# Optimization experiments

Measured on AMD Instinct MI355X. Metric: run time of the kernel, lower is better.

## Reference

```python
import jax, jax.numpy as jnp
import numpy as np

B, N, D_MODEL = 16, 65536, 512
NBUCKETS = 11
BN_EPS = 1e-5
LN_EPS = 1e-5


def setup_inputs() -> dict:
    key = jax.random.key(0)
    ks = jax.random.split(key, 12)
    def w(k, shape, fan_in):
        return jax.random.normal(k, shape, jnp.float32) * (1.0 / np.sqrt(fan_in))
    return {
        "x": jax.random.normal(ks[0], (B, N, 3), jnp.float32),
        "w1": w(ks[1], (3, 64), 3),   "b1": jnp.zeros((64,), jnp.float32),
        "g1": jnp.ones((64,), jnp.float32),  "be1": jnp.zeros((64,), jnp.float32),
        "w2": w(ks[2], (64, 128), 64), "b2": jnp.zeros((128,), jnp.float32),
        "g2": jnp.ones((128,), jnp.float32), "be2": jnp.zeros((128,), jnp.float32),
        "w3": w(ks[3], (128, 256), 128), "b3": jnp.zeros((256,), jnp.float32),
        "g3": jnp.ones((256,), jnp.float32), "be3": jnp.zeros((256,), jnp.float32),
        "wp": w(ks[4], (518, D_MODEL), 518), "bp": jnp.zeros((D_MODEL,), jnp.float32),
        "g_ln": jnp.ones((D_MODEL,), jnp.float32), "b_ln": jnp.zeros((D_MODEL,), jnp.float32),
    }


def _bn(h, g, b):
    # BatchNorm1d in training mode: biased variance over the flattened batch axis
    m = jnp.mean(h, axis=0)
    v = jnp.mean((h - m) ** 2, axis=0)
    return (h - m) * jax.lax.rsqrt(v + BN_EPS) * g + b


def reference(x, w1, b1, g1, be1, w2, b2, g2, be2, w3, b3, g3, be3, wp, bp, g_ln, b_ln):
    Bb, Nn, _ = x.shape
    x_flat = x.reshape(Bb * Nn, 3)
    h = jax.nn.relu(_bn(x_flat @ w1 + b1, g1, be1))
    h = jax.nn.relu(_bn(h @ w2 + b2, g2, be2))
    h = jax.nn.relu(_bn(h @ w3 + b3, g3, be3))
    feat = h.reshape(Bb, Nn, 256)

    # y-bucket histogram means of (x, z) coordinates, vectorized via segment_sum
    y = x[:, :, 1]
    y_min = jnp.min(y, axis=1, keepdims=True)
    y_max = jnp.max(y, axis=1, keepdims=True)
    y_norm = (y - y_min) / (y_max - y_min + 1e-6)
    buckets = jnp.clip((y_norm * 10).astype(jnp.int32), 0, NBUCKETS - 1)  # (B,N) in [0,10]
    seg = (jnp.arange(Bb, dtype=jnp.int32)[:, None] * NBUCKETS + buckets).reshape(-1)
    nseg = Bb * NBUCKETS
    sx = jax.ops.segment_sum(x[:, :, 0].reshape(-1), seg, num_segments=nseg)
    sz = jax.ops.segment_sum(x[:, :, 2].reshape(-1), seg, num_segments=nseg)
    cnt = jax.ops.segment_sum(jnp.ones((Bb * Nn,), jnp.float32), seg, num_segments=nseg)
    denom = jnp.maximum(cnt, 1.0)
    cx = (sx / denom).reshape(Bb, NBUCKETS)
    cz = (sz / denom).reshape(Bb, NBUCKETS)
    x_centers = jnp.take_along_axis(cx, buckets, axis=1)  # (B,N)
    z_centers = jnp.take_along_axis(cz, buckets, axis=1)

    dx = x[:, :, 0] - x_centers
    dz = x[:, :, 2] - z_centers
    theta = jnp.arctan2(dz, dx)
    r = jnp.sqrt(dx ** 2 + dz ** 2)
    spatial = jnp.stack([jnp.sin(theta), jnp.cos(theta), r], axis=-1)  # (B,N,3)

    feat = jnp.concatenate([feat, spatial], axis=-1)  # (B,N,259)
    feat_max = jnp.max(feat, axis=1)
    feat_avg = jnp.mean(feat, axis=1)
    feat_cat = jnp.concatenate([feat_max, feat_avg], axis=1)  # (B,518)

    out = feat_cat @ wp + bp
    mu = jnp.mean(out, axis=-1, keepdims=True)
    var = jnp.mean((out - mu) ** 2, axis=-1, keepdims=True)
    return (out - mu) * jax.lax.rsqrt(var + LN_EPS) * g_ln + b_ln
```

## Files before the change

kernel.cpp:

```cpp
#include <hip/hip_runtime.h>
#include <stdint.h>

#define B_    16
#define N_    65536
#define NPTS  (B_*N_)
#define NBK   11
#define NFEAT 259
#define NF    ((float)NPTS)

typedef float f32x4 __attribute__((ext_vector_type(4)));
typedef short s16x8 __attribute__((ext_vector_type(8)));

enum {
  OFF_YMINF = 16,
  OFF_YMAXF = 32,
  OFF_A1    = 64,
  OFF_C1    = 128,
  OFF_A2    = 192,
  OFF_C2    = 320,
  OFF_CX    = 448,
  OFF_CZ    = 624,
  OFF_A3    = 800,
  OFF_C3    = 1056,
  OFF_PSTR  = 16384,
  OFF_PBKT  = 24576,
  OFF_PH2   = 49152,
  OFF_PH3   = 311296,
  OFF_PPOOL = 835584,
  OFF_PSPA  = 1359872
};

__device__ __forceinline__ float wave_sum(float v){
  #pragma unroll
  for (int m=32;m>=1;m>>=1) v += __shfl_xor(v,m,64);
  return v;
}
__device__ __forceinline__ float wave_max(float v){
  #pragma unroll
  for (int m=32;m>=1;m>>=1) v = fmaxf(v,__shfl_xor(v,m,64));
  return v;
}
__device__ __forceinline__ float wave_min(float v){
  #pragma unroll
  for (int m=32;m>=1;m>>=1) v = fminf(v,__shfl_xor(v,m,64));
  return v;
}
__device__ __forceinline__ unsigned short bf16_bits(float f){
  unsigned u=__float_as_uint(f);
  u += 0x7FFFu + ((u>>16)&1u);
  return (unsigned short)(u>>16);
}

__global__ __launch_bounds__(256) void k_stream0(const float* __restrict__ x,
                                                 float* __restrict__ ws){
  __shared__ float red[4][12];
  const int t=threadIdx.x, l=t&63, w=t>>6;
  const int bid=blockIdx.x;
  const float4* xv=(const float4*)(x + (size_t)bid*2048*3);
  float s0=0,s1=0,s2=0,q00=0,q01=0,q02=0,q11=0,q12=0,q22=0;
  float ymn=3.4e38f, ymx=-3.4e38f;
  #pragma unroll
  for (int i=0;i<2;i++){
    const int vi=(i*256+t)*3;
    const float4 a=xv[vi], b4=xv[vi+1], c=xv[vi+2];
    float X[4]={a.x,a.w,b4.z,c.y};
    float Y[4]={a.y,b4.x,b4.w,c.z};
    float Z[4]={a.z,b4.y,c.x,c.w};
    #pragma unroll
    for (int p=0;p<4;p++){
      s0+=X[p]; s1+=Y[p]; s2+=Z[p];
      q00=fmaf(X[p],X[p],q00); q01=fmaf(X[p],Y[p],q01); q02=fmaf(X[p],Z[p],q02);
      q11=fmaf(Y[p],Y[p],q11); q12=fmaf(Y[p],Z[p],q12); q22=fmaf(Z[p],Z[p],q22);
      ymn=fminf(ymn,Y[p]); ymx=fmaxf(ymx,Y[p]);
    }
  }
  s0=wave_sum(s0); s1=wave_sum(s1); s2=wave_sum(s2);
  q00=wave_sum(q00); q01=wave_sum(q01); q02=wave_sum(q02);
  q11=wave_sum(q11); q12=wave_sum(q12); q22=wave_sum(q22);
  ymn=wave_min(ymn); ymx=wave_max(ymx);
  if (l==0){
    red[w][0]=s0; red[w][1]=s1; red[w][2]=s2;
    red[w][3]=q00; red[w][4]=q01; red[w][5]=q02;
    red[w][6]=q11; red[w][7]=q12; red[w][8]=q22;
    red[w][9]=ymn; red[w][10]=ymx;
  }
  __syncthreads();
  if (t<11){
    const float v0=red[0][t],v1=red[1][t],v2=red[2][t],v3=red[3][t];
    float r;
    if (t==9)       r=fminf(fminf(v0,v1),fminf(v2,v3));
    else if (t==10) r=fmaxf(fmaxf(v0,v1),fmaxf(v2,v3));
    else            r=v0+v1+v2+v3;
    ws[OFF_PSTR+bid*16+t]=r;
  }
}

__global__ void k_finA(const float* __restrict__ w1, const float* __restrict__ b1,
                       const float* __restrict__ gm, const float* __restrict__ bt,
                       float* __restrict__ ws){
  __shared__ float sums[9];
  const int t=threadIdx.x;
  if (t<9){
    float s=0.f;
    #pragma unroll 8
    for (int blk=0;blk<512;blk++) s+=ws[OFF_PSTR+blk*16+t];
    sums[t]=s;
  }
  if (t>=32&&t<48){
    const int b=t-32; float m=3.4e38f;
    #pragma unroll 8
    for (int blk=0;blk<32;blk++) m=fminf(m,ws[OFF_PSTR+(b*32+blk)*16+9]);
    ws[OFF_YMINF+b]=m;
  }
  if (t>=48&&t<64){
    const int b=t-48; float m=-3.4e38f;
    #pragma unroll 8
    for (int blk=0;blk<32;blk++) m=fmaxf(m,ws[OFF_PSTR+(b*32+blk)*16+10]);
    ws[OFF_YMAXF+b]=m;
  }
  __syncthreads();
  if (t<64){
    const float i_n=1.f/NF;
    const float w0=w1[t], wa=w1[64+t], wb=w1[128+t];
    const float ms=(w0*sums[0]+wa*sums[1]+wb*sums[2])*i_n;
    const float es=(w0*w0*sums[3]+wa*wa*sums[6]+wb*wb*sums[8]
                   +2.f*(w0*wa*sums[4]+w0*wb*sums[5]+wa*wb*sums[7]))*i_n;
    const float var=es-ms*ms;
    const float a=gm[t]/sqrtf(var+1e-5f);
    ws[OFF_A1+t]=a; ws[OFF_C1+t]=bt[t]-(ms+b1[t])*a;
  }
}

__global__ __launch_bounds__(256) void k_bucket(const float* __restrict__ x,
                                                float* __restrict__ ws){
  __shared__ float red[4][12];
  const int t=threadIdx.x, l=t&63, w=t>>6;
  const int bid=blockIdx.x, b=bid>>5;
  const float ymn=ws[OFF_YMINF+b], ymx=ws[OFF_YMAXF+b];
  const float4* xv=(const float4*)(x + (size_t)bid*2048*3);
  float sxl[NBK], szl[NBK], cntl[NBK];
  #pragma unroll
  for (int k=0;k<NBK;k++){ sxl[k]=0.f; szl[k]=0.f; cntl[k]=0.f; }
  #pragma unroll
  for (int i=0;i<2;i++){
    const int vi=(i*256+t)*3;
    const float4 a=xv[vi], b4=xv[vi+1], c=xv[vi+2];
    float X[4]={a.x,a.w,b4.z,c.y};
    float Y[4]={a.y,b4.x,b4.w,c.z};
    float Z[4]={a.z,b4.y,c.x,c.w};
    #pragma unroll
    for (int p=0;p<4;p++){
      const float yn=(Y[p]-ymn)/(ymx-ymn+1e-6f);
      int bk=(int)(yn*10.f); bk = bk<0?0:(bk>10?10:bk);
      #pragma unroll
      for (int k=0;k<NBK;k++){
        const bool m=(bk==k);
        sxl[k]+= m?X[p]:0.f; szl[k]+= m?Z[p]:0.f; cntl[k]+= m?1.f:0.f;
      }
    }
  }
  #pragma unroll
  for (int k=0;k<NBK;k++){
    const float s=wave_sum(sxl[k]);
    if (l==0) red[w][k]=s;
  }
  __syncthreads();
  if (t<NBK) ws[OFF_PBKT+bid*36+t]=red[0][t]+red[1][t]+red[2][t]+red[3][t];
  __syncthreads();
  #pragma unroll
  for (int k=0;k<NBK;k++){
    const float z=wave_sum(szl[k]);
    if (l==0) red[w][k]=z;
  }
  __syncthreads();
  if (t<NBK) ws[OFF_PBKT+bid*36+11+t]=red[0][t]+red[1][t]+red[2][t]+red[3][t];
  __syncthreads();
  #pragma unroll
  for (int k=0;k<NBK;k++){
    const float c=wave_sum(cntl[k]);
    if (l==0) red[w][k]=c;
  }
  __syncthreads();
  if (t<NBK) ws[OFF_PBKT+bid*36+22+t]=red[0][t]+red[1][t]+red[2][t]+red[3][t];
}

__global__ void k_finB(const float* __restrict__ gm, const float* __restrict__ bt,
                       float* __restrict__ ws){
  __shared__ float acc[256];
  const int t=threadIdx.x;
  {
    const int col=t&127, part=t>>7;
    float s=0.f;
    #pragma unroll 8
    for (int blk=0;blk<1024;blk++) s+=ws[OFF_PH2+blk*256+part*128+col];
    acc[t]=s;
  }
  __syncthreads();
  if (t<128){
    const float i_n=1.f/NF;
    const float m=acc[t]*i_n;
    const float v=acc[128+t]*i_n-m*m;
    const float a=gm[t]/sqrtf(v+1e-5f);
    ws[OFF_A2+t]=a; ws[OFF_C2+t]=bt[t]-m*a;
  }
  if (t<176){
    const int b=t/NBK, k=t-b*NBK;
    float sx=0.f, sz=0.f, cn=0.f;
    #pragma unroll 8
    for (int blk=0;blk<32;blk++){
      const int p=OFF_PBKT+(b*32+blk)*36;
      sx+=ws[p+k]; sz+=ws[p+11+k]; cn+=ws[p+22+k];
    }
    const float d=fmaxf(cn,1.f);
    ws[OFF_CX+t]=sx/d; ws[OFF_CZ+t]=sz/d;
  }
}

__global__ void k_finC(const float* __restrict__ gm, const float* __restrict__ bt,
                       float* __restrict__ ws){
  __shared__ float acc[512];
  const int t=threadIdx.x;
  {
    const int col=t&255, part=t>>8;
    float s=0.f;
    #pragma unroll 8
    for (int blk=0;blk<1024;blk++) s+=ws[OFF_PH3+blk*512+part*256+col];
    acc[t]=s;
  }
  __syncthreads();
  if (t<256){
    const float i_n=1.f/NF;
    const float m=acc[t]*i_n;
    const float v=acc[256+t]*i_n-m*m;
    const float a=gm[t]/sqrtf(v+1e-5f);
    ws[OFF_A3+t]=a; ws[OFF_C3+t]=bt[t]-m*a;
  }
}

__global__ __launch_bounds__(256) void k_spatial(const float* __restrict__ x,
                                                 float* __restrict__ ws){
  __shared__ float red[4][8];
  const int t=threadIdx.x, l=t&63, w=t>>6;
  const int bid=blockIdx.x, b=bid>>5;
  const float ymn=ws[OFF_YMINF+b], ymx=ws[OFF_YMAXF+b];
  const float4* xv=(const float4*)(x + (size_t)bid*2048*3);
  float mx[3]={-3.4e38f,-3.4e38f,-3.4e38f}, sm[3]={0.f,0.f,0.f};
  #pragma unroll
  for (int i=0;i<2;i++){
    const int vi=(i*256+t)*3;
    const float4 a=xv[vi], b4=xv[vi+1], c=xv[vi+2];
    float X[4]={a.x,a.w,b4.z,c.y};
    float Y[4]={a.y,b4.x,b4.w,c.z};
    float Z[4]={a.z,b4.y,c.x,c.w};
    #pragma unroll
    for (int p=0;p<4;p++){
      const float yn=(Y[p]-ymn)/(ymx-ymn+1e-6f);
      int bk=(int)(yn*10.f); bk = bk<0?0:(bk>10?10:bk);
      const float dx=X[p]-ws[OFF_CX+b*NBK+bk];
      const float dz=Z[p]-ws[OFF_CZ+b*NBK+bk];
      const float r=sqrtf(fmaf(dx,dx,dz*dz));
      const float sn=(r>0.f)?(dz/r):0.f;
      const float cs=(r>0.f)?(dx/r):1.f;
      mx[0]=fmaxf(mx[0],sn); sm[0]+=sn;
      mx[1]=fmaxf(mx[1],cs); sm[1]+=cs;
      mx[2]=fmaxf(mx[2],r);  sm[2]+=r;
    }
  }
  #pragma unroll
  for (int q=0;q<3;q++){
    const float m=wave_max(mx[q]);
    const float s=wave_sum(sm[q]);
    if (l==0){ red[w][q]=m; red[w][4+q]=s; }
  }
  __syncthreads();
  if (t<3)        ws[OFF_PSPA+bid*8+t]  =fmaxf(fmaxf(red[0][t],red[1][t]),fmaxf(red[2][t],red[3][t]));
  else if (t>=4&&t<7){
    const int q=t-4;
    ws[OFF_PSPA+bid*8+4+q]=red[0][4+q]+red[1][4+q]+red[2][4+q]+red[3][4+q];
  }
}

template<int MODE>
__global__ __launch_bounds__(512,1) void k_mlp(
    const float* __restrict__ x,
    const float* __restrict__ w1, const float* __restrict__ b1,
    const float* __restrict__ w2, const float* __restrict__ b2,
    const float* __restrict__ w3, const float* __restrict__ b3,
    float* __restrict__ ws)
{
  __shared__ short g1t[128*72];
  __shared__ short g2t[128*136];
  const int t=threadIdx.x, w=t>>6, l=t&63, lg=l>>4, lr=l&15;
  const int bid=blockIdx.x, b=bid>>5, chunk=bid&31;
  const int ptg=w&1, fgrp=w>>1;
  char* g1c=(char*)g1t; char* g2c=(char*)g2t;

  const int fg=l&7, pj=(l>>3)&7;
  const float* a1=ws+OFF_A1; const float* c1=ws+OFF_C1;
  float w1f[3][8], b1f[8];
  #pragma unroll
  for (int i=0;i<8;i++){
    const int f=8*fg+i; const float a=a1[f];
    #pragma unroll
    for (int q=0;q<3;q++) w1f[q][i]=w1[q*64+f]*a;
    b1f[i]=b1[f]*a+c1[f];
  }

  s16x8 w2f[2][2]; float b2v[2][4];
  #pragma unroll
  for (int j=0;j<2;j++){
    const int col2=(2*fgrp+j)*16+lr;
    const float sc2=(MODE==0)?1.f:ws[OFF_A2+col2];
    #pragma unroll
    for (int kt=0;kt<2;kt++)
      #pragma unroll
      for (int i=0;i<8;i++)
        w2f[j][kt][i]=(short)bf16_bits(w2[(kt*32+8*lg+i)*128+col2]*sc2);
    #pragma unroll
    for (int r=0;r<4;r++){
      const int f2=(2*fgrp+j)*16+4*lg+r;
      b2v[j][r]=(MODE==0)? b2[f2] : (ws[OFF_A2+f2]*b2[f2]+ws[OFF_C2+f2]);
    }
  }

  s16x8 w3f[4][4]; float b3v[4][4];
  if (MODE!=0){
    #pragma unroll
    for (int j=0;j<4;j++){
      const int col3=(4*fgrp+j)*16+lr;
      const float sc3=(MODE==1)?1.f:ws[OFF_A3+col3];
      #pragma unroll
      for (int kt=0;kt<4;kt++)
        #pragma unroll
        for (int i=0;i<8;i++)
          w3f[j][kt][i]=(short)bf16_bits(w3[(kt*32+8*lg+i)*256+col3]*sc3);
      #pragma unroll
      for (int r=0;r<4;r++){
        const int f3=(4*fgrp+j)*16+4*lg+r;
        b3v[j][r]=(MODE==1)? b3[f3] : (ws[OFF_A3+f3]*b3[f3]+ws[OFF_C3+f3]);
      }
    }
  }

  float aS[4][4], aQ[4][4];
  #pragma unroll
  for (int j=0;j<4;j++)
    #pragma unroll
    for (int r=0;r<4;r++){ aS[j][r]=(MODE==2)?-3.4e38f:0.f; aQ[j][r]=0.f; }

  const int base=b*N_+chunk*2048;

  #pragma unroll 1
  for (int it=0; it<16; ++it){
    const int tb=base+it*128;
    #pragma unroll
    for (int s=0;s<2;s++){
      const int pt=16*w+2*pj+s;
      const float x0=x[(tb+pt)*3+0], x1v=x[(tb+pt)*3+1], x2=x[(tb+pt)*3+2];
      unsigned pk[4];
      #pragma unroll
      for (int i=0;i<4;i++){
        float v0=b1f[2*i], v1=b1f[2*i+1];
        v0=fmaf(x0,w1f[0][2*i],v0);  v1=fmaf(x0,w1f[0][2*i+1],v1);
        v0=fmaf(x1v,w1f[1][2*i],v0); v1=fmaf(x1v,w1f[1][2*i+1],v1);
        v0=fmaf(x2,w1f[2][2*i],v0);  v1=fmaf(x2,w1f[2][2*i+1],v1);
        pk[i]=(unsigned)bf16_bits(fmaxf(v0,0.f))|((unsigned)bf16_bits(fmaxf(v1,0.f))<<16);
      }
      *(int4*)(g1c + pt*144 + fg*16) = make_int4(pk[0],pk[1],pk[2],pk[3]);
    }
    __syncthreads();
    #pragma unroll
    for (int pt=0;pt<4;pt++){
      const int row=ptg*64+pt*16+lr;
      const s16x8 bf0=*(const s16x8*)(g1c + row*144 + lg*16);
      const s16x8 bf1=*(const s16x8*)(g1c + row*144 + 64 + lg*16);
      #pragma unroll
      for (int j=0;j<2;j++){
        f32x4 acc={0.f,0.f,0.f,0.f};
        acc=__builtin_amdgcn_mfma_f32_16x16x32_bf16(w2f[j][0],bf0,acc,0,0,0);
        acc=__builtin_amdgcn_mfma_f32_16x16x32_bf16(w2f[j][1],bf1,acc,0,0,0);
        if (MODE==0){
          #pragma unroll
          for (int r=0;r<4;r++){ const float h=acc[r]+b2v[j][r]; aS[j][r]+=h; aQ[j][r]+=h*h; }
        } else {
          const float g0=fmaxf(acc[0]+b2v[j][0],0.f), g1v=fmaxf(acc[1]+b2v[j][1],0.f);
          const float g2v=fmaxf(acc[2]+b2v[j][2],0.f), g3v=fmaxf(acc[3]+b2v[j][3],0.f);
          const unsigned lo=(unsigned)bf16_bits(g0)|((unsigned)bf16_bits(g1v)<<16);
          const unsigned hi=(unsigned)bf16_bits(g2v)|((unsigned)bf16_bits(g3v)<<16);
          *(uint2*)(g2c + row*272 + fgrp*64 + j*32 + lg*8) = make_uint2(lo,hi);
        }
      }
    }
    __syncthreads();
    if (MODE!=0){
      #pragma unroll 1
      for (int pt=0;pt<4;pt++){
        const int row=ptg*64+pt*16+lr;
        const s16x8 bf0=*(const s16x8*)(g2c + row*272 + lg*16);
        const s16x8 bf1=*(const s16x8*)(g2c + row*272 + 64 + lg*16);
        const s16x8 bf2=*(const s16x8*)(g2c + row*272 + 128 + lg*16);
        const s16x8 bf3=*(const s16x8*)(g2c + row*272 + 192 + lg*16);
        #pragma unroll
        for (int j=0;j<4;j++){
          f32x4 a3={0.f,0.f,0.f,0.f};
          a3=__builtin_amdgcn_mfma_f32_16x16x32_bf16(w3f[j][0],bf0,a3,0,0,0);
          a3=__builtin_amdgcn_mfma_f32_16x16x32_bf16(w3f[j][1],bf1,a3,0,0,0);
          a3=__builtin_amdgcn_mfma_f32_16x16x32_bf16(w3f[j][2],bf2,a3,0,0,0);
          a3=__builtin_amdgcn_mfma_f32_16x16x32_bf16(w3f[j][3],bf3,a3,0,0,0);
          #pragma unroll
          for (int r=0;r<4;r++){
            if (MODE==1){
              const float h=a3[r]+b3v[j][r]; aS[j][r]+=h; aQ[j][r]+=h*h;
            } else {
              const float g=fmaxf(a3[r]+b3v[j][r],0.f);
              aS[j][r]=fmaxf(aS[j][r],g); aQ[j][r]+=g;
            }
          }
        }
      }
    }
  }

  const int bid2=bid*2+ptg;
  if (MODE==0){
    #pragma unroll
    for (int j=0;j<2;j++)
      #pragma unroll
      for (int r=0;r<4;r++){
        float s=aS[j][r], q=aQ[j][r];
        #pragma unroll
        for (int m=1;m<16;m<<=1){ s+=__shfl_xor(s,m); q+=__shfl_xor(q,m); }
        if (lr==0){
          const int f2=(2*fgrp+j)*16+4*lg+r;
          ws[OFF_PH2+bid2*256+f2]    =s;
          ws[OFF_PH2+bid2*256+128+f2]=q;
        }
      }
  } else if (MODE==1){
    #pragma unroll
    for (int j=0;j<4;j++)
      #pragma unroll
      for (int r=0;r<4;r++){
        float s=aS[j][r], q=aQ[j][r];
        #pragma unroll
        for (int m=1;m<16;m<<=1){ s+=__shfl_xor(s,m); q+=__shfl_xor(q,m); }
        if (lr==0){
          const int f3=(4*fgrp+j)*16+4*lg+r;
          ws[OFF_PH3+bid2*512+f3]    =s;
          ws[OFF_PH3+bid2*512+256+f3]=q;
        }
      }
  } else {
    #pragma unroll
    for (int j=0;j<4;j++)
      #pragma unroll
      for (int r=0;r<4;r++){
        float mxv=aS[j][r], s=aQ[j][r];
        #pragma unroll
        for (int m=1;m<16;m<<=1){ mxv=fmaxf(mxv,__shfl_xor(mxv,m)); s+=__shfl_xor(s,m); }
        if (lr==0){
          const int f3=(4*fgrp+j)*16+4*lg+r;
          ws[OFF_PPOOL+bid2*512+f3]    =mxv;
          ws[OFF_PPOOL+bid2*512+256+f3]=s;
        }
      }
  }
}

__global__ __launch_bounds__(256) void k_final(
    const float* __restrict__ wp, const float* __restrict__ bp,
    const float* __restrict__ gln, const float* __restrict__ bln,
    float* __restrict__ out, const float* __restrict__ ws)
{
  __shared__ float feat[518];
  __shared__ float red[256];
  const int b=blockIdx.x, t=threadIdx.x;
  {
    float fm=-3.4e38f, fs=0.f;
    #pragma unroll 4
    for (int blk=0;blk<64;blk++){
      const int p=OFF_PPOOL+(b*64+blk)*512;
      fm=fmaxf(fm,ws[p+t]);
      fs+=ws[p+256+t];
    }
    feat[t]=fm; feat[NFEAT+t]=fs*(1.f/65536.f);
  }
  if (t<3){
    float fm=-3.4e38f, fs=0.f;
    #pragma unroll 4
    for (int blk=0;blk<32;blk++){
      const int p=OFF_PSPA+(b*32+blk)*8;
      fm=fmaxf(fm,ws[p+t]);
      fs+=ws[p+4+t];
    }
    feat[256+t]=fm; feat[NFEAT+256+t]=fs*(1.f/65536.f);
  }
  __syncthreads();
  float o0=bp[t], o1=bp[t+256];
  #pragma unroll 4
  for (int i=0;i<518;i++){
    const float f=feat[i];
    o0=fmaf(f, wp[i*512+t],     o0);
    o1=fmaf(f, wp[i*512+t+256], o1);
  }
  red[t]=o0+o1; __syncthreads();
  for (int s=128;s>0;s>>=1){ if (t<s) red[t]+=red[t+s]; __syncthreads(); }
  const float mu=red[0]*(1.f/512.f);
  __syncthreads();
  const float d0=o0-mu, d1=o1-mu;
  red[t]=d0*d0+d1*d1; __syncthreads();
  for (int s=128;s>0;s>>=1){ if (t<s) red[t]+=red[t+s]; __syncthreads(); }
  const float var=red[0]*(1.f/512.f);
  const float rs=1.f/sqrtf(var+1e-5f);
  out[b*512+t]     = d0*rs*gln[t]    +bln[t];
  out[b*512+t+256] = d1*rs*gln[t+256]+bln[t+256];
}

extern "C" void kernel_launch(void* const* d_in, const int* in_sizes, int n_in,
                              void* d_out, int out_size, void* d_ws, size_t ws_size,
                              hipStream_t stream)
{
  const float* x  =(const float*)d_in[0];
  const float* w1 =(const float*)d_in[1];
  const float* b1 =(const float*)d_in[2];
  const float* gm1=(const float*)d_in[3];
  const float* be1=(const float*)d_in[4];
  const float* w2 =(const float*)d_in[5];
  const float* b2 =(const float*)d_in[6];
  const float* gm2=(const float*)d_in[7];
  const float* be2=(const float*)d_in[8];
  const float* w3 =(const float*)d_in[9];
  const float* b3 =(const float*)d_in[10];
  const float* gm3=(const float*)d_in[11];
  const float* be3=(const float*)d_in[12];
  const float* wp =(const float*)d_in[13];
  const float* bp =(const float*)d_in[14];
  const float* gln=(const float*)d_in[15];
  const float* bln=(const float*)d_in[16];
  float* ws=(float*)d_ws;
  float* out=(float*)d_out;

  k_stream0<<<dim3(512),dim3(256),0,stream>>>(x,ws);
  k_finA   <<<dim3(1),  dim3(256),0,stream>>>(w1,b1,gm1,be1,ws);
  k_bucket <<<dim3(512),dim3(256),0,stream>>>(x,ws);
  k_mlp<0> <<<dim3(512),dim3(512),0,stream>>>(x,w1,b1,w2,b2,w3,b3,ws);
  k_finB   <<<dim3(1),  dim3(256),0,stream>>>(gm2,be2,ws);
  k_spatial<<<dim3(512),dim3(256),0,stream>>>(x,ws);
  k_mlp<1> <<<dim3(512),dim3(512),0,stream>>>(x,w1,b1,w2,b2,w3,b3,ws);
  k_finC   <<<dim3(1),  dim3(512),0,stream>>>(gm3,be3,ws);
  k_mlp<2> <<<dim3(512),dim3(512),0,stream>>>(x,w1,b1,w2,b2,w3,b3,ws);
  k_final  <<<dim3(16), dim3(256),0,stream>>>(wp,bp,gln,bln,out,ws);
}
```

Before: 508.6 us.

## Double MLP grid, raise occupancy, prefetch x, fold bias into MFMA accumulators

The three k_mlp passes now launch 1024 blocks of 1024 points each instead of 512 blocks of 2048, with launch bounds allowing two blocks per CU. The workspace layout and the finB, finC and final reductions are resized to match the doubled number of partials. x coordinates for the next tile are prefetched into registers during the current tile, bf16 packing uses the hardware v_cvt_pk_bf16_f32 instruction, and biases seed the MFMA accumulators. The trade-offs are tighter register pressure under the occupancy bound, and the single-block fin kernels must reduce twice as many partials.

New measurement: 623.4 us. 22.6% more time.

```diff
diff --git a/kernel.cpp b/kernel.cpp
--- a/kernel.cpp
+++ b/kernel.cpp
@@ -24,10 +24,10 @@
   OFF_C3    = 1056,
   OFF_PSTR  = 16384,
   OFF_PBKT  = 24576,
+  OFF_PSPA  = 43008,
   OFF_PH2   = 49152,
-  OFF_PH3   = 311296,
-  OFF_PPOOL = 835584,
-  OFF_PSPA  = 1359872
+  OFF_PH3   = 573440,
+  OFF_PPOOL = 1622016
 };
 
 __device__ __forceinline__ float wave_sum(float v){
@@ -49,6 +49,11 @@
   unsigned u=__float_as_uint(f);
   u += 0x7FFFu + ((u>>16)&1u);
   return (unsigned short)(u>>16);
+}
+__device__ __forceinline__ unsigned cvt_pk_bf16(float lo, float hi){
+  unsigned r;
+  asm("v_cvt_pk_bf16_f32 %0, %1, %2" : "=v"(r) : "v"(lo), "v"(hi));
+  return r;
 }
 
 __global__ __launch_bounds__(256) void k_stream0(const float* __restrict__ x,
@@ -192,7 +197,7 @@
     const int col=t&127, part=t>>7;
     float s=0.f;
     #pragma unroll 8
-    for (int blk=0;blk<1024;blk++) s+=ws[OFF_PH2+blk*256+part*128+col];
+    for (int blk=0;blk<2048;blk++) s+=ws[OFF_PH2+blk*256+part*128+col];
     acc[t]=s;
   }
   __syncthreads();
@@ -224,7 +229,7 @@
     const int col=t&255, part=t>>8;
     float s=0.f;
     #pragma unroll 8
-    for (int blk=0;blk<1024;blk++) s+=ws[OFF_PH3+blk*512+part*256+col];
+    for (int blk=0;blk<2048;blk++) s+=ws[OFF_PH3+blk*512+part*256+col];
     acc[t]=s;
   }
   __syncthreads();
@@ -281,7 +286,7 @@
 }
 
 template<int MODE>
-__global__ __launch_bounds__(512,1) void k_mlp(
+__global__ __launch_bounds__(512,2) void k_mlp(
     const float* __restrict__ x,
     const float* __restrict__ w1, const float* __restrict__ b1,
     const float* __restrict__ w2, const float* __restrict__ b2,
@@ -291,7 +296,7 @@
   __shared__ short g1t[128*72];
   __shared__ short g2t[128*136];
   const int t=threadIdx.x, w=t>>6, l=t&63, lg=l>>4, lr=l&15;
-  const int bid=blockIdx.x, b=bid>>5, chunk=bid&31;
+  const int bid=blockIdx.x, b=bid>>6, chunk=bid&63;
   const int ptg=w&1, fgrp=w>>1;
   char* g1c=(char*)g1t; char* g2c=(char*)g2t;
 
@@ -348,15 +353,21 @@
     #pragma unroll
     for (int r=0;r<4;r++){ aS[j][r]=(MODE==2)?-3.4e38f:0.f; aQ[j][r]=0.f; }
 
-  const int base=b*N_+chunk*2048;
+  const int base=b*N_+chunk*1024;
+  const int ptl=16*w+2*pj;
+
+  float c0[3], c1v[3], n0[3], n1[3];
+  {
+    const float* xp=&x[(size_t)(base+ptl)*3];
+    #pragma unroll
+    for (int q=0;q<3;q++){ c0[q]=xp[q]; c1v[q]=xp[3+q]; }
+  }
 
   #pragma unroll 1
-  for (int it=0; it<16; ++it){
-    const int tb=base+it*128;
+  for (int it=0; it<8; ++it){
     #pragma unroll
     for (int s=0;s<2;s++){
-      const int pt=16*w+2*pj+s;
-      const float x0=x[(tb+pt)*3+0], x1v=x[(tb+pt)*3+1], x2=x[(tb+pt)*3+2];
+      const float x0=s?c1v[0]:c0[0], x1v=s?c1v[1]:c0[1], x2=s?c1v[2]:c0[2];
       unsigned pk[4];
       #pragma unroll
       for (int i=0;i<4;i++){
@@ -364,9 +375,14 @@
         v0=fmaf(x0,w1f[0][2*i],v0);  v1=fmaf(x0,w1f[0][2*i+1],v1);
         v0=fmaf(x1v,w1f[1][2*i],v0); v1=fmaf(x1v,w1f[1][2*i+1],v1);
         v0=fmaf(x2,w1f[2][2*i],v0);  v1=fmaf(x2,w1f[2][2*i+1],v1);
-        pk[i]=(unsigned)bf16_bits(fmaxf(v0,0.f))|((unsigned)bf16_bits(fmaxf(v1,0.f))<<16);
-      }
-      *(int4*)(g1c + pt*144 + fg*16) = make_int4(pk[0],pk[1],pk[2],pk[3]);
+        pk[i]=cvt_pk_bf16(fmaxf(v0,0.f),fmaxf(v1,0.f));
+      }
+      *(int4*)(g1c + (ptl+s)*144 + fg*16) = make_int4(pk[0],pk[1],pk[2],pk[3]);
+    }
+    if (it<7){
+      const float* xp=&x[(size_t)(base+(it+1)*128+ptl)*3];
+      #pragma unroll
+      for (int q=0;q<3;q++){ n0[q]=xp[q]; n1[q]=xp[3+q]; }
     }
     __syncthreads();
     #pragma unroll
@@ -376,17 +392,15 @@
       const s16x8 bf1=*(const s16x8*)(g1c + row*144 + 64 + lg*16);
       #pragma unroll
       for (int j=0;j<2;j++){
-        f32x4 acc={0.f,0.f,0.f,0.f};
+        f32x4 acc={b2v[j][0],b2v[j][1],b2v[j][2],b2v[j][3]};
         acc=__builtin_amdgcn_mfma_f32_16x16x32_bf16(w2f[j][0],bf0,acc,0,0,0);
         acc=__builtin_amdgcn_mfma_f32_16x16x32_bf16(w2f[j][1],bf1,acc,0,0,0);
         if (MODE==0){
           #pragma unroll
-          for (int r=0;r<4;r++){ const float h=acc[r]+b2v[j][r]; aS[j][r]+=h; aQ[j][r]+=h*h; }
+          for (int r=0;r<4;r++){ const float h=acc[r]; aS[j][r]+=h; aQ[j][r]=fmaf(h,h,aQ[j][r]); }
         } else {
-          const float g0=fmaxf(acc[0]+b2v[j][0],0.f), g1v=fmaxf(acc[1]+b2v[j][1],0.f);
-          const float g2v=fmaxf(acc[2]+b2v[j][2],0.f), g3v=fmaxf(acc[3]+b2v[j][3],0.f);
-          const unsigned lo=(unsigned)bf16_bits(g0)|((unsigned)bf16_bits(g1v)<<16);
-          const unsigned hi=(unsigned)bf16_bits(g2v)|((unsigned)bf16_bits(g3v)<<16);
+          const unsigned lo=cvt_pk_bf16(fmaxf(acc[0],0.f),fmaxf(acc[1],0.f));
+          const unsigned hi=cvt_pk_bf16(fmaxf(acc[2],0.f),fmaxf(acc[3],0.f));
           *(uint2*)(g2c + row*272 + fgrp*64 + j*32 + lg*8) = make_uint2(lo,hi);
         }
       }
@@ -402,7 +416,7 @@
         const s16x8 bf3=*(const s16x8*)(g2c + row*272 + 192 + lg*16);
         #pragma unroll
         for (int j=0;j<4;j++){
-          f32x4 a3={0.f,0.f,0.f,0.f};
+          f32x4 a3={b3v[j][0],b3v[j][1],b3v[j][2],b3v[j][3]};
           a3=__builtin_amdgcn_mfma_f32_16x16x32_bf16(w3f[j][0],bf0,a3,0,0,0);
           a3=__builtin_amdgcn_mfma_f32_16x16x32_bf16(w3f[j][1],bf1,a3,0,0,0);
           a3=__builtin_amdgcn_mfma_f32_16x16x32_bf16(w3f[j][2],bf2,a3,0,0,0);
@@ -410,15 +424,17 @@
           #pragma unroll
           for (int r=0;r<4;r++){
             if (MODE==1){
-              const float h=a3[r]+b3v[j][r]; aS[j][r]+=h; aQ[j][r]+=h*h;
+              const float h=a3[r]; aS[j][r]+=h; aQ[j][r]=fmaf(h,h,aQ[j][r]);
             } else {
-              const float g=fmaxf(a3[r]+b3v[j][r],0.f);
+              const float g=fmaxf(a3[r],0.f);
               aS[j][r]=fmaxf(aS[j][r],g); aQ[j][r]+=g;
             }
           }
         }
       }
     }
+    #pragma unroll
+    for (int q=0;q<3;q++){ c0[q]=n0[q]; c1v[q]=n1[q]; }
   }
 
   const int bid2=bid*2+ptg;
@@ -478,8 +494,8 @@
   {
     float fm=-3.4e38f, fs=0.f;
     #pragma unroll 4
-    for (int blk=0;blk<64;blk++){
-      const int p=OFF_PPOOL+(b*64+blk)*512;
+    for (int blk=0;blk<128;blk++){
+      const int p=OFF_PPOOL+(b*128+blk)*512;
       fm=fmaxf(fm,ws[p+t]);
       fs+=ws[p+256+t];
     }
@@ -540,14 +556,14 @@
   float* ws=(float*)d_ws;
   float* out=(float*)d_out;
 
-  k_stream0<<<dim3(512),dim3(256),0,stream>>>(x,ws);
-  k_finA   <<<dim3(1),  dim3(256),0,stream>>>(w1,b1,gm1,be1,ws);
-  k_bucket <<<dim3(512),dim3(256),0,stream>>>(x,ws);
-  k_mlp<0> <<<dim3(512),dim3(512),0,stream>>>(x,w1,b1,w2,b2,w3,b3,ws);
-  k_finB   <<<dim3(1),  dim3(256),0,stream>>>(gm2,be2,ws);
-  k_spatial<<<dim3(512),dim3(256),0,stream>>>(x,ws);
-  k_mlp<1> <<<dim3(512),dim3(512),0,stream>>>(x,w1,b1,w2,b2,w3,b3,ws);
-  k_finC   <<<dim3(1),  dim3(512),0,stream>>>(gm3,be3,ws);
-  k_mlp<2> <<<dim3(512),dim3(512),0,stream>>>(x,w1,b1,w2,b2,w3,b3,ws);
-  k_final  <<<dim3(16), dim3(256),0,stream>>>(wp,bp,gln,bln,out,ws);
-}
+  k_stream0<<<dim3(512), dim3(256),0,stream>>>(x,ws);
+  k_finA   <<<dim3(1),   dim3(256),0,stream>>>(w1,b1,gm1,be1,ws);
+  k_bucket <<<dim3(512), dim3(256),0,stream>>>(x,ws);
+  k_mlp<0> <<<dim3(1024),dim3(512),0,stream>>>(x,w1,b1,w2,b2,w3,b3,ws);
+  k_finB   <<<dim3(1),   dim3(256),0,stream>>>(gm2,be2,ws);
+  k_spatial<<<dim3(512), dim3(256),0,stream>>>(x,ws);
+  k_mlp<1> <<<dim3(1024),dim3(512),0,stream>>>(x,w1,b1,w2,b2,w3,b3,ws);
+  k_finC   <<<dim3(1),   dim3(512),0,stream>>>(gm3,be3,ws);
+  k_mlp<2> <<<dim3(1024),dim3(512),0,stream>>>(x,w1,b1,w2,b2,w3,b3,ws);
+  k_final  <<<dim3(16),  dim3(256),0,stream>>>(wp,bp,gln,bln,out,ws);
+}
```
